# Kernel optimization log

Hardware: AMD Instinct MI355X
Metric: run time of the kernel (lower is better)

Reference implementation:

```python
import jax, jax.numpy as jnp
import numpy as np

B, T, C, H = 8, 2048, 1024, 128


def setup_inputs() -> dict:
    key = jax.random.key(0)
    k1, k2, k3, k4 = jax.random.split(key, 4)
    x = jax.random.normal(k1, (B, T, C), dtype=jnp.float32)
    # Linear(n_embd, head_size, bias=False): weight is [head_size, n_embd] in torch,
    # applied as x @ W.T; we store W already transposed as [C, H].
    s = 1.0 / np.sqrt(C)
    Wk = jax.random.normal(k2, (C, H), dtype=jnp.float32) * s
    Wq = jax.random.normal(k3, (C, H), dtype=jnp.float32) * s
    Wv = jax.random.normal(k4, (C, H), dtype=jnp.float32) * s
    return {"x": x, "Wk": Wk, "Wq": Wq, "Wv": Wv}


def reference(x, Wk, Wq, Wv):
    # k, q, v projections
    k = jnp.einsum("btc,ch->bth", x, Wk)
    q = jnp.einsum("btc,ch->bth", x, Wq)
    v = jnp.einsum("btc,ch->bth", x, Wv)
    scale = k.shape[-1] ** -0.5
    wei = jnp.einsum("bqh,bkh->bqk", q, k) * scale  # [B,T,T]
    # causal mask: tril == 0 -> -inf
    Tq = x.shape[1]
    causal = jnp.tril(jnp.ones((Tq, Tq), dtype=bool))
    wei = jnp.where(causal, wei, -jnp.inf)
    wei = jax.nn.softmax(wei, axis=-1)
    # dropout p=0.0 -> identity
    out = jnp.einsum("bqk,bkh->bqh", wei, v)  # [B,T,H]
    return out
```

## Files before the change

kernel.cpp:

```cpp
#include <hip/hip_runtime.h>

typedef unsigned short u16;
typedef __attribute__((ext_vector_type(8))) short bf16x8;
typedef __attribute__((ext_vector_type(4))) float f32x4;
typedef __attribute__((ext_vector_type(4))) unsigned int u32x4;
typedef __attribute__((ext_vector_type(2))) unsigned int u32x2;

#define MFMA16(a, b, c) __builtin_amdgcn_mfma_f32_16x16x32_bf16((a), (b), (c), 0, 0, 0)

static constexpr int Bn = 8, Tn = 2048, Cn = 1024, Hn = 128;

static __device__ __forceinline__ u16 f2bf(float f) {
  union { float f; unsigned u; } v;
  v.f = f;
  unsigned r = v.u + 0x7fffu + ((v.u >> 16) & 1u);
  return (u16)(r >> 16);
}

static __device__ __forceinline__ float bf2f(u16 h) {
  union { unsigned u; float f; } v;
  v.u = ((unsigned)h) << 16;
  return v.f;
}

static __device__ __forceinline__ unsigned pack2(float a, float b) {
  return (unsigned)f2bf(a) | ((unsigned)f2bf(b) << 16);
}

__global__ __launch_bounds__(256) void wt_kernel(const float* __restrict__ Wk,
                                                 const float* __restrict__ Wq,
                                                 const float* __restrict__ Wv,
                                                 u16* __restrict__ Wt) {
  __shared__ u16 tile[64][65];
  const int c0 = blockIdx.x * 64;
  const int h0 = blockIdx.y * 64;
  const int z = blockIdx.z;
  const float* W = (z == 0) ? Wk : (z == 1) ? Wq : Wv;
  u16* dst = Wt + (size_t)z * Hn * Cn;
  const int tx = threadIdx.x & 63;
  const int ty = threadIdx.x >> 6;
#pragma unroll
  for (int i = 0; i < 16; ++i) {
    int r = ty * 16 + i;
    tile[r][tx] = f2bf(W[(size_t)(c0 + r) * Hn + h0 + tx]);
  }
  __syncthreads();
#pragma unroll
  for (int i = 0; i < 16; ++i) {
    int r = ty * 16 + i;
    dst[(size_t)(h0 + r) * Cn + c0 + tx] = tile[tx][r];
  }
}

__global__ __launch_bounds__(512) void proj_kernel(const float* __restrict__ X,
                                                   const u16* __restrict__ Wt,
                                                   u16* __restrict__ Kb,
                                                   u16* __restrict__ Qb,
                                                   u16* __restrict__ Vt) {
  __shared__ u16 Xs[64][72];
  __shared__ u16 Ws[384][72];
  __shared__ u16 Vtmp[128][72];

  const int m0 = blockIdx.x * 64;
  const int tid = threadIdx.x;
  const int w = tid >> 6;
  const int wm = w & 1;
  const int wh = w >> 1;
  const int lane = tid & 63;
  const int l15 = lane & 15, lg = lane >> 4;

  const int trow = tid >> 3;
  const int tcol = (tid & 7) * 8;

  f32x4 acc[6][2] = {};

  for (int kt = 0; kt < Cn; kt += 64) {
    f32x4 x0 = *reinterpret_cast<const f32x4*>(&X[(size_t)(m0 + trow) * Cn + kt + tcol]);
    f32x4 x1 = *reinterpret_cast<const f32x4*>(&X[(size_t)(m0 + trow) * Cn + kt + tcol + 4]);
    bf16x8 wreg[6];
    int wrow[6], wc8[6];
#pragma unroll
    for (int i = 0; i < 6; ++i) {
      const int idx = tid + i * 512;
      wrow[i] = idx >> 3;
      wc8[i] = (idx & 7) * 8;
      wreg[i] = *reinterpret_cast<const bf16x8*>(&Wt[(size_t)wrow[i] * Cn + kt + wc8[i]]);
    }
    __syncthreads();
    union { u16 h[8]; bf16x8 v; } cv;
#pragma unroll
    for (int j = 0; j < 4; ++j) {
      cv.h[j] = f2bf(x0[j]);
      cv.h[4 + j] = f2bf(x1[j]);
    }
    *reinterpret_cast<bf16x8*>(&Xs[trow][tcol]) = cv.v;
#pragma unroll
    for (int i = 0; i < 6; ++i)
      *reinterpret_cast<bf16x8*>(&Ws[wrow[i]][wc8[i]]) = wreg[i];
    __syncthreads();
#pragma unroll
    for (int kk = 0; kk < 2; ++kk) {
      const int ko = kk * 32 + lg * 8;
      bf16x8 wa[6], xb[2];
#pragma unroll
      for (int hf = 0; hf < 6; ++hf)
        wa[hf] = *reinterpret_cast<const bf16x8*>(&Ws[wh * 96 + hf * 16 + l15][ko]);
#pragma unroll
      for (int mf = 0; mf < 2; ++mf)
        xb[mf] = *reinterpret_cast<const bf16x8*>(&Xs[wm * 32 + mf * 16 + l15][ko]);
#pragma unroll
      for (int hf = 0; hf < 6; ++hf)
#pragma unroll
        for (int mf = 0; mf < 2; ++mf)
          acc[hf][mf] = MFMA16(wa[hf], xb[mf], acc[hf][mf]);
    }
  }

#pragma unroll
  for (int hf = 0; hf < 6; ++hf) {
    const int habs = wh * 96 + hf * 16 + lg * 4;
    const int p = habs >> 7;
    const int h = habs & 127;
    const float sc = (p == 1) ? 0.08838834764831845f : 1.0f;
#pragma unroll
    for (int mf = 0; mf < 2; ++mf) {
      const int m = m0 + wm * 32 + mf * 16 + l15;
      const int ml = wm * 32 + mf * 16 + l15;
      if (p == 0) {
        union { u16 h4[4]; u32x2 v; } pk;
#pragma unroll
        for (int r = 0; r < 4; ++r) pk.h4[r] = f2bf(acc[hf][mf][r]);
        *reinterpret_cast<u32x2*>(&Kb[(size_t)m * Hn + h]) = pk.v;
      } else if (p == 1) {
        union { u16 h4[4]; u32x2 v; } pk;
#pragma unroll
        for (int r = 0; r < 4; ++r) pk.h4[r] = f2bf(acc[hf][mf][r] * sc);
        *reinterpret_cast<u32x2*>(&Qb[(size_t)m * Hn + h]) = pk.v;
      } else {
#pragma unroll
        for (int r = 0; r < 4; ++r) Vtmp[h + r][ml] = f2bf(acc[hf][mf][r]);
      }
    }
  }
  __syncthreads();
  {
    const int h = tid >> 2;
    const int c = (tid & 3) * 16;
    const int bV = m0 >> 11;
    const int t0 = m0 & (Tn - 1);
    u32x4 v0 = *reinterpret_cast<const u32x4*>(&Vtmp[h][c]);
    u32x4 v1 = *reinterpret_cast<const u32x4*>(&Vtmp[h][c + 8]);
    u16* dst = &Vt[((size_t)bV * Hn + h) * Tn + t0 + c];
    *reinterpret_cast<u32x4*>(dst) = v0;
    *reinterpret_cast<u32x4*>(dst + 8) = v1;
  }
}

__global__ __launch_bounds__(512) void attn_kernel(const u16* __restrict__ Qb,
                                                   const u16* __restrict__ Kb,
                                                   const u16* __restrict__ Vt,
                                                   float* __restrict__ Out) {
  __shared__ u16 Ks[128][136];
  __shared__ u16 Vs[128][136];
  __shared__ u16 Pl[8][16][72];
  __shared__ u16 Om[8][16][136];
  __shared__ float Ml[8][16][2];

  const int batch = blockIdx.x & 7;
  const int rrank = blockIdx.x >> 3;
  const int q0 = (31 - rrank) << 6;
  const int tid = threadIdx.x;
  const int w = tid >> 6;
  const int sw = w >> 1;
  const int par = w & 1;
  const int lane = tid & 63;
  const int l15 = lane & 15, lg = lane >> 4;

  const size_t bt = (size_t)batch * Tn;
  const int qrow = q0 + sw * 16;
  const int q = qrow + l15;

  bf16x8 qb[4];
#pragma unroll
  for (int kk = 0; kk < 4; ++kk)
    qb[kk] = *reinterpret_cast<const bf16x8*>(&Qb[(bt + q) * Hn + kk * 32 + lg * 8]);

  f32x4 o[8] = {};
  float m_r = -1e30f;
  float l_r = 0.f;

  const int nt = (q0 + 64 + 127) >> 7;

  u32x4 kreg[4], vreg[4];
#pragma unroll
  for (int i = 0; i < 4; ++i) {
    const int idx = tid + i * 512;
    const int row = idx >> 4, c8 = (idx & 15) * 8;
    kreg[i] = *reinterpret_cast<const u32x4*>(&Kb[(bt + row) * Hn + c8]);
    vreg[i] = *reinterpret_cast<const u32x4*>(&Vt[((size_t)batch * Hn + row) * Tn + c8]);
  }

  for (int t = 0; t < nt; ++t) {
    __syncthreads();
#pragma unroll
    for (int i = 0; i < 4; ++i) {
      const int idx = tid + i * 512;
      const int row = idx >> 4, c8 = (idx & 15) * 8;
      *reinterpret_cast<u32x4*>(&Ks[row][c8]) = kreg[i];
      *reinterpret_cast<u32x4*>(&Vs[row][c8]) = vreg[i];
    }
    __syncthreads();
    const int k0 = t << 7;
    if (t + 1 < nt) {
      const int kn = (t + 1) << 7;
#pragma unroll
      for (int i = 0; i < 4; ++i) {
        const int idx = tid + i * 512;
        const int row = idx >> 4, c8 = (idx & 15) * 8;
        kreg[i] = *reinterpret_cast<const u32x4*>(&Kb[(bt + kn + row) * Hn + c8]);
        vreg[i] = *reinterpret_cast<const u32x4*>(&Vt[((size_t)batch * Hn + row) * Tn + kn + c8]);
      }
    }

    const int kbase = k0 + par * 64;
    if (kbase <= qrow) {
      f32x4 s[4] = {};
#pragma unroll
      for (int nf = 0; nf < 4; ++nf) {
#pragma unroll
        for (int kk = 0; kk < 4; ++kk) {
          bf16x8 ka = *reinterpret_cast<const bf16x8*>(
              &Ks[par * 64 + nf * 16 + l15][kk * 32 + lg * 8]);
          s[nf] = MFMA16(ka, qb[kk], s[nf]);
        }
      }

      if (kbase + 63 > qrow) {
#pragma unroll
        for (int nf = 0; nf < 4; ++nf)
#pragma unroll
          for (int r = 0; r < 4; ++r)
            if (kbase + nf * 16 + lg * 4 + r > q) s[nf][r] = -1e30f;
      }

      float mx = -1e30f;
#pragma unroll
      for (int nf = 0; nf < 4; ++nf)
#pragma unroll
        for (int r = 0; r < 4; ++r) mx = fmaxf(mx, s[nf][r]);
      mx = fmaxf(mx, __shfl_xor(mx, 16));
      mx = fmaxf(mx, __shfl_xor(mx, 32));
      const float mn = fmaxf(m_r, mx);
      const float sc = __expf(m_r - mn);
      float rs = 0.f;
#pragma unroll
      for (int nf = 0; nf < 4; ++nf)
#pragma unroll
        for (int r = 0; r < 4; ++r) {
          s[nf][r] = __expf(s[nf][r] - mn);
          rs += s[nf][r];
        }
      rs += __shfl_xor(rs, 16);
      rs += __shfl_xor(rs, 32);
      l_r = l_r * sc + rs;
      m_r = mn;
#pragma unroll
      for (int n = 0; n < 8; ++n) o[n] *= sc;

#pragma unroll
      for (int nf = 0; nf < 4; ++nf) {
        u32x2 pv;
        pv.x = pack2(s[nf][0], s[nf][1]);
        pv.y = pack2(s[nf][2], s[nf][3]);
        *reinterpret_cast<u32x2*>(&Pl[w][l15][nf * 16 + lg * 4]) = pv;
      }
      asm volatile("s_waitcnt lgkmcnt(0)" ::: "memory");
      __builtin_amdgcn_sched_barrier(0);
      bf16x8 pb[2];
#pragma unroll
      for (int ks = 0; ks < 2; ++ks)
        pb[ks] = *reinterpret_cast<const bf16x8*>(&Pl[w][l15][ks * 32 + lg * 8]);

#pragma unroll
      for (int n = 0; n < 8; ++n) {
#pragma unroll
        for (int ks = 0; ks < 2; ++ks) {
          bf16x8 va = *reinterpret_cast<const bf16x8*>(
              &Vs[n * 16 + l15][par * 64 + ks * 32 + lg * 8]);
          o[n] = MFMA16(va, pb[ks], o[n]);
        }
      }
    }
  }

#pragma unroll
  for (int n = 0; n < 8; ++n) {
    u32x2 ov;
    ov.x = pack2(o[n][0], o[n][1]);
    ov.y = pack2(o[n][2], o[n][3]);
    *reinterpret_cast<u32x2*>(&Om[w][l15][n * 16 + lg * 4]) = ov;
  }
  if (lg == 0) {
    Ml[w][l15][0] = m_r;
    Ml[w][l15][1] = l_r;
  }
  __syncthreads();

  {
    const int row = tid >> 3;
    const int h0 = (tid & 7) * 16;
    const int s_ = row >> 4;
    const int r16 = row & 15;
    const int w0 = s_ * 2, w1 = w0 + 1;
    const float m0v = Ml[w0][r16][0], l0v = Ml[w0][r16][1];
    const float m1v = Ml[w1][r16][0], l1v = Ml[w1][r16][1];
    const float M = fmaxf(m0v, m1v);
    const float e0 = __expf(m0v - M), e1 = __expf(m1v - M);
    const float inv = 1.0f / (l0v * e0 + l1v * e1);
    u32x4 a0 = *reinterpret_cast<const u32x4*>(&Om[w0][r16][h0]);
    u32x4 a1 = *reinterpret_cast<const u32x4*>(&Om[w0][r16][h0 + 8]);
    u32x4 b0 = *reinterpret_cast<const u32x4*>(&Om[w1][r16][h0]);
    u32x4 b1 = *reinterpret_cast<const u32x4*>(&Om[w1][r16][h0 + 8]);
    float outv[16];
#pragma unroll
    for (int j = 0; j < 4; ++j) {
      outv[2 * j]     = (e0 * bf2f((u16)(a0[j] & 0xffffu)) + e1 * bf2f((u16)(b0[j] & 0xffffu))) * inv;
      outv[2 * j + 1] = (e0 * bf2f((u16)(a0[j] >> 16))     + e1 * bf2f((u16)(b0[j] >> 16))) * inv;
      outv[8 + 2 * j]     = (e0 * bf2f((u16)(a1[j] & 0xffffu)) + e1 * bf2f((u16)(b1[j] & 0xffffu))) * inv;
      outv[8 + 2 * j + 1] = (e0 * bf2f((u16)(a1[j] >> 16))     + e1 * bf2f((u16)(b1[j] >> 16))) * inv;
    }
    float* op = &Out[(bt + q0 + row) * Hn + h0];
#pragma unroll
    for (int j = 0; j < 4; ++j)
      *reinterpret_cast<f32x4*>(op + j * 4) = *reinterpret_cast<const f32x4*>(&outv[j * 4]);
  }
}

extern "C" void kernel_launch(void* const* d_in, const int* in_sizes, int n_in,
                              void* d_out, int out_size, void* d_ws, size_t ws_size,
                              hipStream_t stream) {
  const float* X = (const float*)d_in[0];
  const float* Wk = (const float*)d_in[1];
  const float* Wq = (const float*)d_in[2];
  const float* Wv = (const float*)d_in[3];

  char* ws = (char*)d_ws;
  u16* Wt = (u16*)(ws);
  u16* Kb = (u16*)(ws + 786432);
  u16* Qb = (u16*)(ws + 786432 + 4194304);
  u16* Vt = (u16*)(ws + 786432 + 2 * 4194304);
  float* Out = (float*)d_out;

  wt_kernel<<<dim3(16, 2, 3), 256, 0, stream>>>(Wk, Wq, Wv, Wt);
  proj_kernel<<<dim3(256), 512, 0, stream>>>(X, Wt, Kb, Qb, Vt);
  attn_kernel<<<dim3(Bn * 32), 512, 0, stream>>>(Qb, Kb, Vt, Out);
}
```

Measured before the change: 77.20 us.

## Double-buffer K/V tiles in attention and restructure projection with direct W loads

The attention kernel now keeps two K/V tiles in one shared buffer, so staging the next tile and prefetching the one after overlap with compute and each iteration needs one barrier instead of two. The projection kernel drops the shared W tile: each warp loads its 48 weight rows straight from global into registers, software-pipelined two k-steps deep, and computes all 64 rows of the X tile. V is written directly to the transposed output with scattered 2-byte stores instead of going through a shared transpose buffer. The scattered V stores and the larger shared footprint (about 157KB) may cost bandwidth and occupancy.

```diff
diff --git a/kernel.cpp b/kernel.cpp
--- a/kernel.cpp
+++ b/kernel.cpp
@@ -58,101 +58,104 @@
                                                    u16* __restrict__ Qb,
                                                    u16* __restrict__ Vt) {
   __shared__ u16 Xs[64][72];
-  __shared__ u16 Ws[384][72];
-  __shared__ u16 Vtmp[128][72];
 
   const int m0 = blockIdx.x * 64;
   const int tid = threadIdx.x;
   const int w = tid >> 6;
-  const int wm = w & 1;
-  const int wh = w >> 1;
   const int lane = tid & 63;
   const int l15 = lane & 15, lg = lane >> 4;
-
-  const int trow = tid >> 3;
-  const int tcol = (tid & 7) * 8;
-
-  f32x4 acc[6][2] = {};
-
-  for (int kt = 0; kt < Cn; kt += 64) {
-    f32x4 x0 = *reinterpret_cast<const f32x4*>(&X[(size_t)(m0 + trow) * Cn + kt + tcol]);
-    f32x4 x1 = *reinterpret_cast<const f32x4*>(&X[(size_t)(m0 + trow) * Cn + kt + tcol + 4]);
-    bf16x8 wreg[6];
-    int wrow[6], wc8[6];
-#pragma unroll
-    for (int i = 0; i < 6; ++i) {
-      const int idx = tid + i * 512;
-      wrow[i] = idx >> 3;
-      wc8[i] = (idx & 7) * 8;
-      wreg[i] = *reinterpret_cast<const bf16x8*>(&Wt[(size_t)wrow[i] * Cn + kt + wc8[i]]);
-    }
-    __syncthreads();
-    union { u16 h[8]; bf16x8 v; } cv;
-#pragma unroll
-    for (int j = 0; j < 4; ++j) {
-      cv.h[j] = f2bf(x0[j]);
-      cv.h[4 + j] = f2bf(x1[j]);
-    }
-    *reinterpret_cast<bf16x8*>(&Xs[trow][tcol]) = cv.v;
-#pragma unroll
-    for (int i = 0; i < 6; ++i)
-      *reinterpret_cast<bf16x8*>(&Ws[wrow[i]][wc8[i]]) = wreg[i];
-    __syncthreads();
-#pragma unroll
-    for (int kk = 0; kk < 2; ++kk) {
-      const int ko = kk * 32 + lg * 8;
-      bf16x8 wa[6], xb[2];
-#pragma unroll
-      for (int hf = 0; hf < 6; ++hf)
-        wa[hf] = *reinterpret_cast<const bf16x8*>(&Ws[wh * 96 + hf * 16 + l15][ko]);
-#pragma unroll
-      for (int mf = 0; mf < 2; ++mf)
-        xb[mf] = *reinterpret_cast<const bf16x8*>(&Xs[wm * 32 + mf * 16 + l15][ko]);
-#pragma unroll
-      for (int hf = 0; hf < 6; ++hf)
-#pragma unroll
-        for (int mf = 0; mf < 2; ++mf)
-          acc[hf][mf] = MFMA16(wa[hf], xb[mf], acc[hf][mf]);
-    }
-  }
-
-#pragma unroll
-  for (int hf = 0; hf < 6; ++hf) {
-    const int habs = wh * 96 + hf * 16 + lg * 4;
+  const int lgo8 = lg * 8;
+
+  const float* xbase = X + (size_t)(m0 + (tid >> 3)) * Cn + (tid & 7) * 8;
+  size_t wrow[3];
+#pragma unroll
+  for (int hf = 0; hf < 3; ++hf)
+    wrow[hf] = (size_t)(w * 48 + hf * 16 + l15) * Cn;
+
+  f32x4 acc[3][4] = {};
+
+  f32x4 xA0, xA1, xB0, xB1;
+  bf16x8 wA[6], wB[6];
+
+#define PROJ_LOADX(R0, R1, KT)                                        \
+  R0 = *reinterpret_cast<const f32x4*>(xbase + (KT));                 \
+  R1 = *reinterpret_cast<const f32x4*>(xbase + (KT) + 4);
+
+#define PROJ_LOADW(WR, KT)                                            \
+  _Pragma("unroll")                                                   \
+  for (int c = 0; c < 6; ++c)                                         \
+    WR[c] = *reinterpret_cast<const bf16x8*>(                         \
+        &Wt[wrow[c >> 1] + (KT) + (c & 1) * 32 + lgo8]);
+
+#define PROJ_STAGE(R0, R1)                                            \
+  {                                                                   \
+    union { u16 h[8]; bf16x8 v; } cv;                                 \
+    _Pragma("unroll")                                                 \
+    for (int j = 0; j < 4; ++j) {                                     \
+      cv.h[j] = f2bf(R0[j]);                                          \
+      cv.h[4 + j] = f2bf(R1[j]);                                      \
+    }                                                                 \
+    *reinterpret_cast<bf16x8*>(&Xs[tid >> 3][(tid & 7) * 8]) = cv.v;  \
+  }
+
+#define PROJ_COMP(WR)                                                 \
+  _Pragma("unroll")                                                   \
+  for (int kk = 0; kk < 2; ++kk) {                                    \
+    bf16x8 xb[4];                                                     \
+    _Pragma("unroll")                                                 \
+    for (int mf = 0; mf < 4; ++mf)                                    \
+      xb[mf] = *reinterpret_cast<const bf16x8*>(                      \
+          &Xs[mf * 16 + l15][kk * 32 + lgo8]);                        \
+    _Pragma("unroll")                                                 \
+    for (int hf = 0; hf < 3; ++hf)                                    \
+      _Pragma("unroll")                                               \
+      for (int mf = 0; mf < 4; ++mf)                                  \
+        acc[hf][mf] = MFMA16(WR[hf * 2 + (kk)], xb[mf], acc[hf][mf]); \
+  }
+
+  PROJ_LOADX(xA0, xA1, 0)
+  PROJ_LOADW(wA, 0)
+
+  for (int kt = 0; kt < Cn; kt += 128) {
+    __syncthreads();
+    PROJ_STAGE(xA0, xA1)
+    __syncthreads();
+    PROJ_LOADX(xB0, xB1, kt + 64)
+    PROJ_LOADW(wB, kt + 64)
+    PROJ_COMP(wA)
+    __syncthreads();
+    PROJ_STAGE(xB0, xB1)
+    __syncthreads();
+    if (kt + 128 < Cn) {
+      PROJ_LOADX(xA0, xA1, kt + 128)
+      PROJ_LOADW(wA, kt + 128)
+    }
+    PROJ_COMP(wB)
+  }
+
+#pragma unroll
+  for (int hf = 0; hf < 3; ++hf) {
+    const int habs = w * 48 + hf * 16 + lg * 4;
     const int p = habs >> 7;
     const int h = habs & 127;
     const float sc = (p == 1) ? 0.08838834764831845f : 1.0f;
 #pragma unroll
-    for (int mf = 0; mf < 2; ++mf) {
-      const int m = m0 + wm * 32 + mf * 16 + l15;
-      const int ml = wm * 32 + mf * 16 + l15;
+    for (int mf = 0; mf < 4; ++mf) {
+      const int m = m0 + mf * 16 + l15;
+      union { u16 h4[4]; u32x2 v; } pk;
+#pragma unroll
+      for (int r = 0; r < 4; ++r) pk.h4[r] = f2bf(acc[hf][mf][r] * sc);
       if (p == 0) {
-        union { u16 h4[4]; u32x2 v; } pk;
-#pragma unroll
-        for (int r = 0; r < 4; ++r) pk.h4[r] = f2bf(acc[hf][mf][r]);
         *reinterpret_cast<u32x2*>(&Kb[(size_t)m * Hn + h]) = pk.v;
       } else if (p == 1) {
-        union { u16 h4[4]; u32x2 v; } pk;
-#pragma unroll
-        for (int r = 0; r < 4; ++r) pk.h4[r] = f2bf(acc[hf][mf][r] * sc);
         *reinterpret_cast<u32x2*>(&Qb[(size_t)m * Hn + h]) = pk.v;
       } else {
-#pragma unroll
-        for (int r = 0; r < 4; ++r) Vtmp[h + r][ml] = f2bf(acc[hf][mf][r]);
-      }
-    }
-  }
-  __syncthreads();
-  {
-    const int h = tid >> 2;
-    const int c = (tid & 3) * 16;
-    const int bV = m0 >> 11;
-    const int t0 = m0 & (Tn - 1);
-    u32x4 v0 = *reinterpret_cast<const u32x4*>(&Vtmp[h][c]);
-    u32x4 v1 = *reinterpret_cast<const u32x4*>(&Vtmp[h][c + 8]);
-    u16* dst = &Vt[((size_t)bV * Hn + h) * Tn + t0 + c];
-    *reinterpret_cast<u32x4*>(dst) = v0;
-    *reinterpret_cast<u32x4*>(dst + 8) = v1;
+        const int b = m >> 11, t = m & (Tn - 1);
+#pragma unroll
+        for (int r = 0; r < 4; ++r)
+          Vt[((size_t)b * Hn + h + r) * Tn + t] = pk.h4[r];
+      }
+    }
   }
 }
 
@@ -160,10 +163,7 @@
                                                    const u16* __restrict__ Kb,
                                                    const u16* __restrict__ Vt,
                                                    float* __restrict__ Out) {
-  __shared__ u16 Ks[128][136];
-  __shared__ u16 Vs[128][136];
-  __shared__ u16 Pl[8][16][72];
-  __shared__ u16 Om[8][16][136];
+  __shared__ u16 SM[78848];
   __shared__ float Ml[8][16][2];
 
   const int batch = blockIdx.x & 7;
@@ -191,46 +191,49 @@
 
   const int nt = (q0 + 64 + 127) >> 7;
 
+  const int srow = tid >> 4;
+  const int sc8 = (tid & 15) * 8;
+  (void)srow; (void)sc8;
+
   u32x4 kreg[4], vreg[4];
-#pragma unroll
-  for (int i = 0; i < 4; ++i) {
-    const int idx = tid + i * 512;
-    const int row = idx >> 4, c8 = (idx & 15) * 8;
-    kreg[i] = *reinterpret_cast<const u32x4*>(&Kb[(bt + row) * Hn + c8]);
-    vreg[i] = *reinterpret_cast<const u32x4*>(&Vt[((size_t)batch * Hn + row) * Tn + c8]);
-  }
+#define ATTN_LOAD(KN)                                                          \
+  _Pragma("unroll")                                                            \
+  for (int i = 0; i < 4; ++i) {                                                \
+    const int idx = tid + i * 512;                                             \
+    const int row = idx >> 4, c8 = (idx & 15) * 8;                             \
+    kreg[i] = *reinterpret_cast<const u32x4*>(&Kb[(bt + (KN) + row) * Hn + c8]); \
+    vreg[i] = *reinterpret_cast<const u32x4*>(                                 \
+        &Vt[((size_t)batch * Hn + row) * Tn + (KN) + c8]);                     \
+  }
+
+#define ATTN_STAGE(BUF)                                                        \
+  _Pragma("unroll")                                                            \
+  for (int i = 0; i < 4; ++i) {                                                \
+    const int idx = tid + i * 512;                                             \
+    const int row = idx >> 4, c8 = (idx & 15) * 8;                             \
+    *reinterpret_cast<u32x4*>(&SM[(BUF) * 34816 + row * 136 + c8]) = kreg[i];  \
+    *reinterpret_cast<u32x4*>(&SM[(BUF) * 34816 + 17408 + row * 136 + c8]) = vreg[i]; \
+  }
+
+  ATTN_LOAD(0)
+  ATTN_STAGE(0)
+  if (nt > 1) ATTN_LOAD(128)
+  __syncthreads();
 
   for (int t = 0; t < nt; ++t) {
-    __syncthreads();
-#pragma unroll
-    for (int i = 0; i < 4; ++i) {
-      const int idx = tid + i * 512;
-      const int row = idx >> 4, c8 = (idx & 15) * 8;
-      *reinterpret_cast<u32x4*>(&Ks[row][c8]) = kreg[i];
-      *reinterpret_cast<u32x4*>(&Vs[row][c8]) = vreg[i];
-    }
-    __syncthreads();
+    const int cur = t & 1;
     const int k0 = t << 7;
-    if (t + 1 < nt) {
-      const int kn = (t + 1) << 7;
-#pragma unroll
-      for (int i = 0; i < 4; ++i) {
-        const int idx = tid + i * 512;
-        const int row = idx >> 4, c8 = (idx & 15) * 8;
-        kreg[i] = *reinterpret_cast<const u32x4*>(&Kb[(bt + kn + row) * Hn + c8]);
-        vreg[i] = *reinterpret_cast<const u32x4*>(&Vt[((size_t)batch * Hn + row) * Tn + kn + c8]);
-      }
-    }
-
     const int kbase = k0 + par * 64;
     if (kbase <= qrow) {
+      const u16* KsB = &SM[cur * 34816];
+      const u16* VsB = &SM[cur * 34816 + 17408];
       f32x4 s[4] = {};
 #pragma unroll
       for (int nf = 0; nf < 4; ++nf) {
 #pragma unroll
         for (int kk = 0; kk < 4; ++kk) {
           bf16x8 ka = *reinterpret_cast<const bf16x8*>(
-              &Ks[par * 64 + nf * 16 + l15][kk * 32 + lg * 8]);
+              &KsB[(par * 64 + nf * 16 + l15) * 136 + kk * 32 + lg * 8]);
           s[nf] = MFMA16(ka, qb[kk], s[nf]);
         }
       }
@@ -251,7 +254,7 @@
       mx = fmaxf(mx, __shfl_xor(mx, 16));
       mx = fmaxf(mx, __shfl_xor(mx, 32));
       const float mn = fmaxf(m_r, mx);
-      const float sc = __expf(m_r - mn);
+      const float scv = __expf(m_r - mn);
       float rs = 0.f;
 #pragma unroll
       for (int nf = 0; nf < 4; ++nf)
@@ -262,35 +265,42 @@
         }
       rs += __shfl_xor(rs, 16);
       rs += __shfl_xor(rs, 32);
-      l_r = l_r * sc + rs;
+      l_r = l_r * scv + rs;
       m_r = mn;
 #pragma unroll
-      for (int n = 0; n < 8; ++n) o[n] *= sc;
-
+      for (int n = 0; n < 8; ++n) o[n] *= scv;
+
+      u16* PlW = &SM[69632 + w * 1152];
 #pragma unroll
       for (int nf = 0; nf < 4; ++nf) {
         u32x2 pv;
         pv.x = pack2(s[nf][0], s[nf][1]);
         pv.y = pack2(s[nf][2], s[nf][3]);
-        *reinterpret_cast<u32x2*>(&Pl[w][l15][nf * 16 + lg * 4]) = pv;
+        *reinterpret_cast<u32x2*>(&PlW[l15 * 72 + nf * 16 + lg * 4]) = pv;
       }
       asm volatile("s_waitcnt lgkmcnt(0)" ::: "memory");
       __builtin_amdgcn_sched_barrier(0);
       bf16x8 pb[2];
 #pragma unroll
       for (int ks = 0; ks < 2; ++ks)
-        pb[ks] = *reinterpret_cast<const bf16x8*>(&Pl[w][l15][ks * 32 + lg * 8]);
+        pb[ks] = *reinterpret_cast<const bf16x8*>(&PlW[l15 * 72 + ks * 32 + lg * 8]);
 
 #pragma unroll
       for (int n = 0; n < 8; ++n) {
 #pragma unroll
         for (int ks = 0; ks < 2; ++ks) {
           bf16x8 va = *reinterpret_cast<const bf16x8*>(
-              &Vs[n * 16 + l15][par * 64 + ks * 32 + lg * 8]);
+              &VsB[(n * 16 + l15) * 136 + par * 64 + ks * 32 + lg * 8]);
           o[n] = MFMA16(va, pb[ks], o[n]);
         }
       }
     }
+
+    if (t + 1 < nt) {
+      ATTN_STAGE(cur ^ 1)
+      if (t + 2 < nt) ATTN_LOAD((t + 2) << 7)
+    }
+    __syncthreads();
   }
 
 #pragma unroll
@@ -298,7 +308,7 @@
     u32x2 ov;
     ov.x = pack2(o[n][0], o[n][1]);
     ov.y = pack2(o[n][2], o[n][3]);
-    *reinterpret_cast<u32x2*>(&Om[w][l15][n * 16 + lg * 4]) = ov;
+    *reinterpret_cast<u32x2*>(&SM[w * 2176 + l15 * 136 + n * 16 + lg * 4]) = ov;
   }
   if (lg == 0) {
     Ml[w][l15][0] = m_r;
@@ -317,10 +327,12 @@
     const float M = fmaxf(m0v, m1v);
     const float e0 = __expf(m0v - M), e1 = __expf(m1v - M);
     const float inv = 1.0f / (l0v * e0 + l1v * e1);
-    u32x4 a0 = *reinterpret_cast<const u32x4*>(&Om[w0][r16][h0]);
-    u32x4 a1 = *reinterpret_cast<const u32x4*>(&Om[w0][r16][h0 + 8]);
-    u32x4 b0 = *reinterpret_cast<const u32x4*>(&Om[w1][r16][h0]);
-    u32x4 b1 = *reinterpret_cast<const u32x4*>(&Om[w1][r16][h0 + 8]);
+    const u16* Oa = &SM[w0 * 2176 + r16 * 136 + h0];
+    const u16* Ob = &SM[w1 * 2176 + r16 * 136 + h0];
+    u32x4 a0 = *reinterpret_cast<const u32x4*>(Oa);
+    u32x4 a1 = *reinterpret_cast<const u32x4*>(Oa + 8);
+    u32x4 b0 = *reinterpret_cast<const u32x4*>(Ob);
+    u32x4 b1 = *reinterpret_cast<const u32x4*>(Ob + 8);
     float outv[16];
 #pragma unroll
     for (int j = 0; j < 4; ++j) {
```

After: 81.04 us. +5.0%, slower.
